# Kernel optimization log

Hardware: AMD Instinct MI355X
Metric: run time of the kernel (lower is better)

Reference implementation:

```python
import jax, jax.numpy as jnp
import numpy as np

N = 131072      # total sentences
D = 512         # d_MLP_size == bag_feature_dim
D_ATT = 256
N_HEAD = 4
N_CLASSES = 53
BAG_SIZE = 16
N_BAGS = N // BAG_SIZE


def setup_inputs() -> dict:
    key = jax.random.key(0)
    k_x, k_w1, k_w2, k_wc, k_bc = jax.random.split(key, 5)
    x = jax.random.normal(k_x, (N, D), dtype=jnp.float32)
    # equal-sized bags (ragged boundaries collapsed to segment ids)
    seg_ids = (jnp.arange(N, dtype=jnp.int32) // BAG_SIZE).astype(jnp.int32)
    # parameters, stored (in, out); math identical to nn.Linear(x @ W.T)
    W1 = jax.random.normal(k_w1, (D, D_ATT), dtype=jnp.float32) / np.sqrt(D)
    W2 = jax.random.normal(k_w2, (D_ATT, N_HEAD), dtype=jnp.float32) / np.sqrt(D_ATT)
    Wc = jax.random.normal(k_wc, (D, N_CLASSES), dtype=jnp.float32) / np.sqrt(D)
    bc = jax.random.normal(k_bc, (N_CLASSES,), dtype=jnp.float32) * 0.01
    return {"x": x, "W1": W1, "W2": W2, "Wc": Wc, "bc": bc,
            "seg_ids": seg_ids, "n_bags": N_BAGS}


def reference(x, W1, W2, Wc, bc, seg_ids, n_bags):
    # scores per sentence per head: tanh(x W1) W2  -> (N, H)
    s = jnp.tanh(x @ W1) @ W2
    # segment-wise (per-bag) softmax over sentences, per head
    smax = jax.ops.segment_max(s, seg_ids, num_segments=n_bags)      # (B, H)
    e = jnp.exp(s - smax[seg_ids])                                   # (N, H)
    denom = jax.ops.segment_sum(e, seg_ids, num_segments=n_bags)     # (B, H)
    alpha = e / denom[seg_ids]                                       # (N, H)
    # torch: mean over heads of (H, n_i) attention, then alpha @ x
    w = jnp.mean(alpha, axis=1)                                      # (N,)
    bag_repr = jax.ops.segment_sum(w[:, None] * x, seg_ids,
                                   num_segments=n_bags)              # (B, D)
    # dropout is identity in eval / p=0
    logits = bag_repr @ Wc + bc                                      # (B, C)
    return logits
```

## Files before the change

### kernel.cpp

```cpp
#include <hip/hip_runtime.h>
#include <hip/hip_bf16.h>

#define N_TOTAL   131072
#define D         512
#define D_ATT     256
#define N_HEAD    4
#define N_CLASSES 53
#define BAG       16
#define M_TILE    64
#define THREADS   256
#define N_BLOCKS  (N_TOTAL / M_TILE)
#define BK        32
#define K_ITERS   (D / BK)
#define NC_PAD    64

typedef __attribute__((ext_vector_type(8))) short bf16x8;
typedef __attribute__((ext_vector_type(4))) float f32x4;

__device__ __forceinline__ unsigned short f2bf(float f) {
    __hip_bfloat16 h = __float2bfloat16(f);
    return *reinterpret_cast<unsigned short*>(&h);
}
__device__ __forceinline__ unsigned int pack_bf(float a, float b) {
    unsigned int ua = __float_as_uint(a) + 0x8000u;
    unsigned int ub = __float_as_uint(b) + 0x8000u;
    return __builtin_amdgcn_perm(ub, ua, 0x07060302u);
}

typedef __attribute__((address_space(3))) unsigned char lds_u8;
typedef __attribute__((address_space(1))) const unsigned char g_u8;
__device__ __forceinline__ void gload_lds16(const void* g, void* l) {
    __builtin_amdgcn_global_load_lds((g_u8*)g, (lds_u8*)l, 16, 0, 0);
}

__global__ void prep_kernel(const float* __restrict__ W1, const float* __restrict__ Wc,
                            unsigned short* __restrict__ W1T, unsigned short* __restrict__ WcTb) {
    int tid = blockIdx.x * 256 + threadIdx.x;
    if (tid < D * D_ATT) {
        int k = tid >> 8;
        int n = tid & 255;
        W1T[n * D + k] = f2bf(W1[k * D_ATT + n]);
    } else {
        int t2 = tid - D * D_ATT;
        int n = t2 >> 9;
        int k = t2 & 511;
        WcTb[n * D + k] = (n < N_CLASSES) ? f2bf(Wc[k * N_CLASSES + n])
                                          : (unsigned short)0;
    }
}

__device__ __forceinline__ bf16x8 read_a_frag(const unsigned char* ldsAbase, int r, int quad) {
    const int m = r & 7;
    const float4 u0 = *reinterpret_cast<const float4*>(
        ldsAbase + (size_t)(r * 8 + ((quad * 2)     ^ m)) * 16);
    const float4 u1 = *reinterpret_cast<const float4*>(
        ldsAbase + (size_t)(r * 8 + ((quad * 2 + 1) ^ m)) * 16);
    bf16x8 o;
    unsigned int* op = reinterpret_cast<unsigned int*>(&o);
    op[0] = pack_bf(u0.x, u0.y);
    op[1] = pack_bf(u0.z, u0.w);
    op[2] = pack_bf(u1.x, u1.y);
    op[3] = pack_bf(u1.z, u1.w);
    return o;
}
__device__ __forceinline__ bf16x8 read_b_frag(const unsigned char* base, int n, int quad) {
    const int pos = quad ^ ((n >> 1) & 3);
    return *reinterpret_cast<const bf16x8*>(base + (size_t)(n * 4 + pos) * 16);
}

__global__ void __launch_bounds__(THREADS, 3)
fused_kernel(const float* __restrict__ x,
             const unsigned short* __restrict__ W1T,
             const unsigned short* __restrict__ WcTb,
             const float* __restrict__ W2,
             const float* __restrict__ bc,
             float* __restrict__ out)
{
    __shared__ __align__(16) unsigned char ldsA[M_TILE * BK * 4];
    __shared__ __align__(16) unsigned char ldsB[D_ATT * BK * 2];
    __shared__ __align__(16) unsigned char ldsC[NC_PAD * BK * 2];
    __shared__ float ldsSp[4][M_TILE][N_HEAD];
    __shared__ float ldsS[M_TILE][N_HEAD];
    __shared__ float ldsM[4][N_HEAD];
    __shared__ float ldsDen[4][N_HEAD];
    __shared__ float ldsW[M_TILE];

    const int tid  = threadIdx.x;
    const int wave = tid >> 6;
    const int lane = tid & 63;
    const int quad = lane >> 4;
    const int l16  = lane & 15;
    const int row_base = blockIdx.x * M_TILE;

    const char* gA[2]; unsigned lA[2];
    #pragma unroll
    for (int i = 0; i < 2; ++i) {
        int c = tid + 256 * i, r = c >> 3, p = c & 7, j = p ^ (r & 7);
        gA[i] = (const char*)(x + (size_t)(row_base + r) * D + j * 4);
        lA[i] = c * 16;
    }
    const char* gB[4]; unsigned lB[4];
    #pragma unroll
    for (int i = 0; i < 4; ++i) {
        int c = tid + 256 * i, n = c >> 2, p = c & 3, j = p ^ ((n >> 1) & 3);
        gB[i] = (const char*)(W1T + (size_t)n * D + j * 8);
        lB[i] = c * 16;
    }
    const char* gC; unsigned lC;
    {
        int c = tid, n = c >> 2, p = c & 3, j = p ^ ((n >> 1) & 3);
        gC = (const char*)(WcTb + (size_t)n * D + j * 8);
        lC = c * 16;
    }

    f32x4 acc[4][4] = {};
    f32x4 accY[4]   = {};

    for (int kt = 0; kt < K_ITERS; ++kt) {
        const size_t ao = (size_t)kt * (BK * 4);
        const size_t bo = (size_t)kt * (BK * 2);
        gload_lds16(gA[0] + ao, ldsA + lA[0]);
        gload_lds16(gA[1] + ao, ldsA + lA[1]);
        gload_lds16(gB[0] + bo, ldsB + lB[0]);
        gload_lds16(gB[1] + bo, ldsB + lB[1]);
        gload_lds16(gB[2] + bo, ldsB + lB[2]);
        gload_lds16(gB[3] + bo, ldsB + lB[3]);
        gload_lds16(gC + bo,    ldsC + lC);
        __syncthreads();

        bf16x8 afr[4];
        #pragma unroll
        for (int mi = 0; mi < 4; ++mi)
            afr[mi] = read_a_frag(ldsA, mi * 16 + l16, quad);
        bf16x8 bfr[4];
        #pragma unroll
        for (int ni = 0; ni < 4; ++ni)
            bfr[ni] = read_b_frag(ldsB, wave * 64 + ni * 16 + l16, quad);
        #pragma unroll
        for (int mi = 0; mi < 4; ++mi)
            #pragma unroll
            for (int ni = 0; ni < 4; ++ni)
                acc[mi][ni] = __builtin_amdgcn_mfma_f32_16x16x32_bf16(
                    afr[mi], bfr[ni], acc[mi][ni], 0, 0, 0);

        bf16x8 ay = read_a_frag(ldsA, wave * 16 + l16, quad);
        #pragma unroll
        for (int ni = 0; ni < 4; ++ni) {
            bf16x8 cf = read_b_frag(ldsC, ni * 16 + l16, quad);
            accY[ni] = __builtin_amdgcn_mfma_f32_16x16x32_bf16(
                ay, cf, accY[ni], 0, 0, 0);
        }
        __syncthreads();
    }

    {
        float4 w2r[4];
        #pragma unroll
        for (int ni = 0; ni < 4; ++ni)
            w2r[ni] = *reinterpret_cast<const float4*>(&W2[(wave * 64 + ni * 16 + l16) * 4]);

        #pragma unroll
        for (int mi = 0; mi < 4; ++mi) {
            float sp[4][4] = {};
            #pragma unroll
            for (int ni = 0; ni < 4; ++ni) {
                f32x4 v = acc[mi][ni];
                #pragma unroll
                for (int r = 0; r < 4; ++r) {
                    float e = __expf(2.f * v[r]);
                    float t = 1.f - 2.f / (e + 1.f);
                    sp[r][0] += t * w2r[ni].x;
                    sp[r][1] += t * w2r[ni].y;
                    sp[r][2] += t * w2r[ni].z;
                    sp[r][3] += t * w2r[ni].w;
                }
            }
            #pragma unroll
            for (int msk = 1; msk < 16; msk <<= 1)
                #pragma unroll
                for (int r = 0; r < 4; ++r)
                    #pragma unroll
                    for (int h = 0; h < 4; ++h)
                        sp[r][h] += __shfl_xor(sp[r][h], msk, 64);
            if (l16 == 0) {
                #pragma unroll
                for (int r = 0; r < 4; ++r) {
                    int row = mi * 16 + quad * 4 + r;
                    float4 v4 = {sp[r][0], sp[r][1], sp[r][2], sp[r][3]};
                    *reinterpret_cast<float4*>(&ldsSp[wave][row][0]) = v4;
                }
            }
        }
    }
    __syncthreads();

    {
        int row = tid >> 2, h = tid & 3;
        ldsS[row][h] = ldsSp[0][row][h] + ldsSp[1][row][h]
                     + ldsSp[2][row][h] + ldsSp[3][row][h];
    }
    __syncthreads();

    if (tid < 4 * N_HEAD) {
        int bag = tid >> 2, head = tid & 3;
        float m = -1e30f;
        for (int i = 0; i < BAG; ++i)
            m = fmaxf(m, ldsS[bag * BAG + i][head]);
        float den = 0.f;
        for (int i = 0; i < BAG; ++i)
            den += __expf(ldsS[bag * BAG + i][head] - m);
        ldsM[bag][head] = m;
        ldsDen[bag][head] = 1.f / den;
    }
    __syncthreads();
    if (tid < M_TILE) {
        int row = tid, bag = row >> 4;
        float w = 0.f;
        #pragma unroll
        for (int h = 0; h < 4; ++h)
            w += __expf(ldsS[row][h] - ldsM[bag][h]) * ldsDen[bag][h];
        ldsW[row] = 0.25f * w;
    }
    __syncthreads();

    {
        float p[4];
        #pragma unroll
        for (int ni = 0; ni < 4; ++ni) {
            f32x4 v = accY[ni];
            float s = 0.f;
            #pragma unroll
            for (int r = 0; r < 4; ++r)
                s += ldsW[wave * 16 + quad * 4 + r] * v[r];
            s += __shfl_xor(s, 16, 64);
            s += __shfl_xor(s, 32, 64);
            p[ni] = s;
        }
        if (quad == 0) {
            size_t bag = (size_t)blockIdx.x * 4 + wave;
            #pragma unroll
            for (int ni = 0; ni < 4; ++ni) {
                int c = ni * 16 + l16;
                if (c < N_CLASSES)
                    out[bag * N_CLASSES + c] = p[ni] + bc[c];
            }
        }
    }
}

extern "C" void kernel_launch(void* const* d_in, const int* in_sizes, int n_in,
                              void* d_out, int out_size, void* d_ws, size_t ws_size,
                              hipStream_t stream) {
    const float* x  = (const float*)d_in[0];
    const float* W1 = (const float*)d_in[1];
    const float* W2 = (const float*)d_in[2];
    const float* Wc = (const float*)d_in[3];
    const float* bc = (const float*)d_in[4];

    unsigned short* W1T  = (unsigned short*)d_ws;
    unsigned short* WcTb = (unsigned short*)((char*)d_ws + 262144);

    prep_kernel<<<dim3(640), dim3(256), 0, stream>>>(W1, Wc, W1T, WcTb);

    fused_kernel<<<dim3(N_BLOCKS), dim3(THREADS), 0, stream>>>(
        x, W1T, WcTb, W2, bc, (float*)d_out);
}
```

Measured before the change: 407.3 us.

## Double-buffer LDS tiles with register-staged bf16 A conversion and unrolled K loop

Replaces the single-buffered K loop with a double-buffered pipeline. The next W1/Wc tile is loaded straight into LDS while the current one is computed, and x is prefetched two steps ahead into registers, packed to bf16 once and stored to LDS with a padded stride. This removes one barrier per iteration and the per-wave repeated fp32-to-bf16 conversion on LDS reads, and it halves the A LDS footprint. The Y GEMM is remapped so each wave handles one 16-class slice and reuses the A fragments already loaded for the attention GEMM. The costs are more registers for the prefetch, a larger LDS allocation that may limit occupancy, and reuse of the staging buffers for the epilogue.

```diff
diff --git a/kernel.cpp b/kernel.cpp
--- a/kernel.cpp
+++ b/kernel.cpp
@@ -12,7 +12,6 @@
 #define N_BLOCKS  (N_TOTAL / M_TILE)
 #define BK        32
 #define K_ITERS   (D / BK)
-#define NC_PAD    64
 
 typedef __attribute__((ext_vector_type(8))) short bf16x8;
 typedef __attribute__((ext_vector_type(4))) float f32x4;
@@ -29,9 +28,7 @@
 
 typedef __attribute__((address_space(3))) unsigned char lds_u8;
 typedef __attribute__((address_space(1))) const unsigned char g_u8;
-__device__ __forceinline__ void gload_lds16(const void* g, void* l) {
-    __builtin_amdgcn_global_load_lds((g_u8*)g, (lds_u8*)l, 16, 0, 0);
-}
+#define GLD16(G, L) __builtin_amdgcn_global_load_lds((g_u8*)(G), (lds_u8*)(L), 16, 0, 0)
 
 __global__ void prep_kernel(const float* __restrict__ W1, const float* __restrict__ Wc,
                             unsigned short* __restrict__ W1T, unsigned short* __restrict__ WcTb) {
@@ -49,23 +46,37 @@
     }
 }
 
-__device__ __forceinline__ bf16x8 read_a_frag(const unsigned char* ldsAbase, int r, int quad) {
-    const int m = r & 7;
-    const float4 u0 = *reinterpret_cast<const float4*>(
-        ldsAbase + (size_t)(r * 8 + ((quad * 2)     ^ m)) * 16);
-    const float4 u1 = *reinterpret_cast<const float4*>(
-        ldsAbase + (size_t)(r * 8 + ((quad * 2 + 1) ^ m)) * 16);
-    bf16x8 o;
-    unsigned int* op = reinterpret_cast<unsigned int*>(&o);
-    op[0] = pack_bf(u0.x, u0.y);
-    op[1] = pack_bf(u0.z, u0.w);
-    op[2] = pack_bf(u1.x, u1.y);
-    op[3] = pack_bf(u1.z, u1.w);
-    return o;
+#define A_STRIDE 80
+#define A_TILE_B (M_TILE * A_STRIDE)
+__device__ __forceinline__ bf16x8 read_a16(const unsigned char* base, int r, int quad) {
+    return *reinterpret_cast<const bf16x8*>(base + (unsigned)(r * A_STRIDE + quad * 16));
 }
 __device__ __forceinline__ bf16x8 read_b_frag(const unsigned char* base, int n, int quad) {
     const int pos = quad ^ ((n >> 1) & 3);
-    return *reinterpret_cast<const bf16x8*>(base + (size_t)(n * 4 + pos) * 16);
+    return *reinterpret_cast<const bf16x8*>(base + (unsigned)(n * 4 + pos) * 16u);
+}
+
+__device__ __forceinline__ void compute_tile(
+        const unsigned char* bA, const unsigned char* bB, const unsigned char* bC,
+        int wave, int l16, int quad, f32x4 acc[4][4], f32x4* accY) {
+    bf16x8 afr[4];
+    #pragma unroll
+    for (int mi = 0; mi < 4; ++mi)
+        afr[mi] = read_a16(bA, mi * 16 + l16, quad);
+    bf16x8 bfr[4];
+    #pragma unroll
+    for (int ni = 0; ni < 4; ++ni)
+        bfr[ni] = read_b_frag(bB, wave * 64 + ni * 16 + l16, quad);
+    #pragma unroll
+    for (int mi = 0; mi < 4; ++mi)
+        #pragma unroll
+        for (int ni = 0; ni < 4; ++ni)
+            acc[mi][ni] = __builtin_amdgcn_mfma_f32_16x16x32_bf16(
+                afr[mi], bfr[ni], acc[mi][ni], 0, 0, 0);
+    bf16x8 cf = read_b_frag(bC, wave * 16 + l16, quad);
+    #pragma unroll
+    for (int mi = 0; mi < 4; ++mi)
+        accY[mi] = __builtin_amdgcn_mfma_f32_16x16x32_bf16(afr[mi], cf, accY[mi], 0, 0, 0);
 }
 
 __global__ void __launch_bounds__(THREADS, 3)
@@ -76,14 +87,13 @@
              const float* __restrict__ bc,
              float* __restrict__ out)
 {
-    __shared__ __align__(16) unsigned char ldsA[M_TILE * BK * 4];
-    __shared__ __align__(16) unsigned char ldsB[D_ATT * BK * 2];
-    __shared__ __align__(16) unsigned char ldsC[NC_PAD * BK * 2];
-    __shared__ float ldsSp[4][M_TILE][N_HEAD];
-    __shared__ float ldsS[M_TILE][N_HEAD];
-    __shared__ float ldsM[4][N_HEAD];
-    __shared__ float ldsDen[4][N_HEAD];
-    __shared__ float ldsW[M_TILE];
+    __shared__ __align__(16) unsigned char lds[51200];
+    unsigned char* bA0 = lds;
+    unsigned char* bA1 = lds + 5120;
+    unsigned char* bB0 = lds + 10240;
+    unsigned char* bB1 = lds + 26624;
+    unsigned char* bC0 = lds + 43008;
+    unsigned char* bC1 = lds + 47104;
 
     const int tid  = threadIdx.x;
     const int wave = tid >> 6;
@@ -92,66 +102,78 @@
     const int l16  = lane & 15;
     const int row_base = blockIdx.x * M_TILE;
 
-    const char* gA[2]; unsigned lA[2];
-    #pragma unroll
-    for (int i = 0; i < 2; ++i) {
-        int c = tid + 256 * i, r = c >> 3, p = c & 7, j = p ^ (r & 7);
-        gA[i] = (const char*)(x + (size_t)(row_base + r) * D + j * 4);
-        lA[i] = c * 16;
-    }
-    const char* gB[4]; unsigned lB[4];
-    #pragma unroll
-    for (int i = 0; i < 4; ++i) {
-        int c = tid + 256 * i, n = c >> 2, p = c & 3, j = p ^ ((n >> 1) & 3);
-        gB[i] = (const char*)(W1T + (size_t)n * D + j * 8);
-        lB[i] = c * 16;
-    }
-    const char* gC; unsigned lC;
-    {
-        int c = tid, n = c >> 2, p = c & 3, j = p ^ ((n >> 1) & 3);
-        gC = (const char*)(WcTb + (size_t)n * D + j * 8);
-        lC = c * 16;
+    const int r_st = tid >> 2;
+    const int j_st = tid & 3;
+    const float* gA = x + (size_t)(row_base + r_st) * D + j_st * 8;
+    const unsigned aWoff = (unsigned)(r_st * A_STRIDE + j_st * 16);
+
+    const char* gB0; const char* gC0; unsigned lB0;
+    {
+        int n = tid >> 2, p = tid & 3, j = p ^ ((n >> 1) & 3);
+        gB0 = (const char*)(W1T  + (size_t)n * D + j * 8);
+        gC0 = (const char*)(WcTb + (size_t)n * D + j * 8);
+        lB0 = (unsigned)tid * 16u;
     }
 
     f32x4 acc[4][4] = {};
     f32x4 accY[4]   = {};
-
-    for (int kt = 0; kt < K_ITERS; ++kt) {
-        const size_t ao = (size_t)kt * (BK * 4);
-        const size_t bo = (size_t)kt * (BK * 2);
-        gload_lds16(gA[0] + ao, ldsA + lA[0]);
-        gload_lds16(gA[1] + ao, ldsA + lA[1]);
-        gload_lds16(gB[0] + bo, ldsB + lB[0]);
-        gload_lds16(gB[1] + bo, ldsB + lB[1]);
-        gload_lds16(gB[2] + bo, ldsB + lB[2]);
-        gload_lds16(gB[3] + bo, ldsB + lB[3]);
-        gload_lds16(gC + bo,    ldsC + lC);
-        __syncthreads();
-
-        bf16x8 afr[4];
-        #pragma unroll
-        for (int mi = 0; mi < 4; ++mi)
-            afr[mi] = read_a_frag(ldsA, mi * 16 + l16, quad);
-        bf16x8 bfr[4];
-        #pragma unroll
-        for (int ni = 0; ni < 4; ++ni)
-            bfr[ni] = read_b_frag(ldsB, wave * 64 + ni * 16 + l16, quad);
-        #pragma unroll
-        for (int mi = 0; mi < 4; ++mi)
-            #pragma unroll
-            for (int ni = 0; ni < 4; ++ni)
-                acc[mi][ni] = __builtin_amdgcn_mfma_f32_16x16x32_bf16(
-                    afr[mi], bfr[ni], acc[mi][ni], 0, 0, 0);
-
-        bf16x8 ay = read_a_frag(ldsA, wave * 16 + l16, quad);
-        #pragma unroll
-        for (int ni = 0; ni < 4; ++ni) {
-            bf16x8 cf = read_b_frag(ldsC, ni * 16 + l16, quad);
-            accY[ni] = __builtin_amdgcn_mfma_f32_16x16x32_bf16(
-                ay, cf, accY[ni], 0, 0, 0);
-        }
-        __syncthreads();
-    }
+    float4 aR0a, aR0b, aR1a, aR1b;
+
+#define LOAD_A(RA, RB, KT) do { \
+        (RA) = *reinterpret_cast<const float4*>(gA + (KT) * BK);     \
+        (RB) = *reinterpret_cast<const float4*>(gA + (KT) * BK + 4); \
+    } while (0)
+
+#define PACK_A(DST, RA, RB) do { \
+        uint4 _pw; \
+        _pw.x = pack_bf((RA).x, (RA).y); \
+        _pw.y = pack_bf((RA).z, (RA).w); \
+        _pw.z = pack_bf((RB).x, (RB).y); \
+        _pw.w = pack_bf((RB).z, (RB).w); \
+        *reinterpret_cast<uint4*>((DST) + aWoff) = _pw; \
+    } while (0)
+
+#define STAGE_BC(DB, DC, KT) do { \
+        GLD16(gB0 +          (KT) * 64, (DB) + lB0);          \
+        GLD16(gB0 +  65536 + (KT) * 64, (DB) + lB0 +  4096);  \
+        GLD16(gB0 + 131072 + (KT) * 64, (DB) + lB0 +  8192);  \
+        GLD16(gB0 + 196608 + (KT) * 64, (DB) + lB0 + 12288);  \
+        GLD16(gC0 +          (KT) * 64, (DC) + lC0);          \
+    } while (0)
+    const unsigned lC0 = lB0;
+
+#define BODY(KT) do { \
+        STAGE_BC(((KT) & 1) ? bB0 : bB1, ((KT) & 1) ? bC0 : bC1, (KT) + 1); \
+        if (((KT) & 1) == 0) { \
+            PACK_A(bA1, aR1a, aR1b); \
+            if ((KT) + 2 <= 15) LOAD_A(aR0a, aR0b, (KT) + 2); \
+        } else { \
+            PACK_A(bA0, aR0a, aR0b); \
+            if ((KT) + 2 <= 15) LOAD_A(aR1a, aR1b, (KT) + 2); \
+        } \
+        compute_tile(((KT) & 1) ? bA1 : bA0, ((KT) & 1) ? bB1 : bB0, \
+                     ((KT) & 1) ? bC1 : bC0, wave, l16, quad, acc, accY); \
+        __syncthreads(); \
+    } while (0)
+
+    LOAD_A(aR0a, aR0b, 0);
+    STAGE_BC(bB0, bC0, 0);
+    LOAD_A(aR1a, aR1b, 1);
+    PACK_A(bA0, aR0a, aR0b);
+    __syncthreads();
+
+    BODY(0);  BODY(1);  BODY(2);  BODY(3);
+    BODY(4);  BODY(5);  BODY(6);  BODY(7);
+    BODY(8);  BODY(9);  BODY(10); BODY(11);
+    BODY(12); BODY(13); BODY(14);
+
+    compute_tile(bA1, bB1, bC1, wave, l16, quad, acc, accY);
+
+    float (*ldsSp)[M_TILE][N_HEAD] = reinterpret_cast<float (*)[M_TILE][N_HEAD]>(lds);
+    float (*ldsS)[N_HEAD]   = reinterpret_cast<float (*)[N_HEAD]>(lds + 5120);
+    float (*ldsM)[N_HEAD]   = reinterpret_cast<float (*)[N_HEAD]>(lds + 6144);
+    float (*ldsDen)[N_HEAD] = reinterpret_cast<float (*)[N_HEAD]>(lds + 6208);
+    float* ldsW             = reinterpret_cast<float*>(lds + 6272);
 
     {
         float4 w2r[4];
@@ -226,26 +248,32 @@
     {
         float p[4];
         #pragma unroll
-        for (int ni = 0; ni < 4; ++ni) {
-            f32x4 v = accY[ni];
+        for (int mi = 0; mi < 4; ++mi) {
+            f32x4 v = accY[mi];
             float s = 0.f;
             #pragma unroll
             for (int r = 0; r < 4; ++r)
-                s += ldsW[wave * 16 + quad * 4 + r] * v[r];
+                s += ldsW[mi * 16 + quad * 4 + r] * v[r];
             s += __shfl_xor(s, 16, 64);
             s += __shfl_xor(s, 32, 64);
-            p[ni] = s;
+            p[mi] = s;
         }
         if (quad == 0) {
-            size_t bag = (size_t)blockIdx.x * 4 + wave;
-            #pragma unroll
-            for (int ni = 0; ni < 4; ++ni) {
-                int c = ni * 16 + l16;
-                if (c < N_CLASSES)
-                    out[bag * N_CLASSES + c] = p[ni] + bc[c];
+            int c = wave * 16 + l16;
+            if (c < N_CLASSES) {
+                float b = bc[c];
+                #pragma unroll
+                for (int mi = 0; mi < 4; ++mi) {
+                    size_t bag = (size_t)blockIdx.x * 4 + mi;
+                    out[bag * N_CLASSES + c] = p[mi] + b;
+                }
             }
         }
     }
+#undef BODY
+#undef STAGE_BC
+#undef PACK_A
+#undef LOAD_A
 }
 
 extern "C" void kernel_launch(void* const* d_in, const int* in_sizes, int n_in,
```

Measured after the change: 407.0 us. About the same (-0.1%).
